# Optimization experiments

Measured on AMD Instinct MI355X. Metric: run time of the kernel, lower is better.

Reference implementation:

```python
import jax, jax.numpy as jnp
import numpy as np

N_TOKEN = 64
H = 16
D = 1024
D_K = 64
D_V = 64
S3 = 30  # 3 * S, number of gated leading positions
GATE_INIT = 10.0


def setup_inputs() -> dict:
    key = jax.random.key(0)
    ks = jax.random.split(key, 8)
    B, L = 32, 2048
    x = jax.random.normal(ks[0], (B, L, D), dtype=jnp.float32)
    q_init = (1.0 / D_K) ** 0.5
    q_tok = jax.random.uniform(ks[1], (1, N_TOKEN, D), minval=-q_init, maxval=q_init, dtype=jnp.float32)
    scale = 0.02
    Wq = jax.random.normal(ks[2], (D, H * D_K), dtype=jnp.float32) * scale
    Wk = jax.random.normal(ks[3], (D, H * D_K), dtype=jnp.float32) * scale
    Wv = jax.random.normal(ks[4], (D, H * D_V), dtype=jnp.float32) * scale
    Wfc = jax.random.normal(ks[5], (H * D_V, D), dtype=jnp.float32) * scale
    gate_logit = -jnp.ones((S3,), dtype=jnp.float32) * GATE_INIT  # matches module init
    gamma = jnp.ones((D,), dtype=jnp.float32)
    beta = jnp.zeros((D,), dtype=jnp.float32)
    return {"x": x, "q_tok": q_tok, "Wq": Wq, "Wk": Wk, "Wv": Wv, "Wfc": Wfc,
            "gate_logit": gate_logit, "gamma": gamma, "beta": beta}


def reference(x, q_tok, Wq, Wk, Wv, Wfc, gate_logit, gamma, beta):
    # x: [B, L, D]; q_tok: [1, n_token, D]. Dropout is identity (eval mode).
    B, L, _ = x.shape
    temp = D_K ** 0.5

    # Cumulative-product gate over the first 30 positions (the torch for-loop).
    gate = jnp.cumprod(1.0 - jax.nn.sigmoid(gate_logit))  # [30]
    x1 = x.at[:, :S3].multiply(gate[None, :, None])

    q = (q_tok @ Wq).reshape(N_TOKEN, H, D_K)          # [n, H, dk]
    k = (x @ Wk).reshape(B, L, H, D_K)                  # [B, L, H, dk]
    v = (x1 @ Wv).reshape(B, L, H, D_V)                 # [B, L, H, dv]

    scores = jnp.einsum('nhd,blhd->bhnl', q / temp, k)  # [B, H, n, L]
    attn = jax.nn.softmax(scores, axis=-1)
    out = jnp.einsum('bhnl,blhd->bnhd', attn, v).reshape(B, N_TOKEN, H * D_V)

    out = out @ Wfc + q_tok                              # residual with query tokens

    # LayerNorm over last dim, eps=1e-6
    mu = jnp.mean(out, axis=-1, keepdims=True)
    var = jnp.mean(jnp.square(out - mu), axis=-1, keepdims=True)
    out = (out - mu) * jax.lax.rsqrt(var + 1e-6) * gamma + beta
    return out
```

## Files before the change

### kernel.cpp

```cpp
#include <hip/hip_runtime.h>
#include <stdint.h>

typedef unsigned short u16;
typedef short bf16x8 __attribute__((ext_vector_type(8)));
typedef float f32x4 __attribute__((ext_vector_type(4)));

__device__ __forceinline__ u16 f2b(float f) {
  uint32_t u = __builtin_bit_cast(uint32_t, f);
  u += 0x7fffu + ((u >> 16) & 1u);
  return (u16)(u >> 16);
}

__device__ __forceinline__ void gload_lds16(const void* g, void* l) {
  __builtin_amdgcn_global_load_lds(
      (const __attribute__((address_space(1))) void*)g,
      (__attribute__((address_space(3))) void*)l, 16, 0, 0);
}

__global__ __launch_bounds__(256) void cvt_kernel(const float* __restrict__ src,
                                                  u16* __restrict__ dst, int n8) {
  int stride = gridDim.x * 256;
  for (int idx = blockIdx.x * 256 + threadIdx.x; idx < n8; idx += stride) {
    int64_t i = (int64_t)idx * 8;
    float4 a = *(const float4*)(src + i);
    float4 b = *(const float4*)(src + i + 4);
    union { u16 u[8]; bf16x8 v; } o;
    o.u[0] = f2b(a.x); o.u[1] = f2b(a.y); o.u[2] = f2b(a.z); o.u[3] = f2b(a.w);
    o.u[4] = f2b(b.x); o.u[5] = f2b(b.y); o.u[6] = f2b(b.z); o.u[7] = f2b(b.w);
    *(bf16x8*)(dst + i) = o.v;
  }
}

__global__ __launch_bounds__(256) void transpose_all_kernel(
    const float* __restrict__ Wk, const float* __restrict__ Wv,
    const float* __restrict__ Wfc, const float* __restrict__ Wq,
    u16* __restrict__ wkvT, u16* __restrict__ wfcT, u16* __restrict__ wqT,
    const float* __restrict__ gl, float* __restrict__ gate) {
  if (blockIdx.x == 0 && threadIdx.x == 0) {
    float g = 1.0f;
    for (int i = 0; i < 30; ++i) {
      float s = 1.0f / (1.0f + __expf(-gl[i]));
      g *= (1.0f - s);
      gate[i] = g;
    }
  }
  __shared__ float ls[64][65];
  int which = blockIdx.x >> 8;
  int tile = blockIdx.x & 255;
  const float* src = (which == 0) ? Wk : (which == 1) ? Wv : (which == 2) ? Wfc : Wq;
  u16* dst = (which == 0) ? wkvT : (which == 1) ? (wkvT + 1024 * 1024)
           : (which == 2) ? wfcT : wqT;
  int t = threadIdx.x;
  int bx = tile & 15;
  int by = tile >> 4;
  int r0 = by * 64, c0 = bx * 64;
  int tr = t >> 6, tc = t & 63;
#pragma unroll
  for (int i = 0; i < 16; ++i)
    ls[tr + i * 4][tc] = src[(int64_t)(r0 + tr + i * 4) * 1024 + c0 + tc];
  __syncthreads();
#pragma unroll
  for (int i = 0; i < 16; ++i)
    dst[(int64_t)(c0 + tr + i * 4) * 1024 + r0 + tc] = f2b(ls[tc][tr + i * 4]);
}

__global__ __launch_bounds__(256, 4) void q_gemm_kernel(
    const u16* __restrict__ qtokb, const u16* __restrict__ wqT, u16* __restrict__ qb) {
  __shared__ u16 As[4096];
  __shared__ u16 Bs[8192];
  int n0 = blockIdx.x * 128;
  int t = threadIdx.x, w = t >> 6, lane = t & 63;
  int wn = w * 32;
  f32x4 acc[2][4] = {};
  int l3 = lane >> 3;
  int colE = ((lane & 7) ^ l3) * 8;
  const u16* aS = qtokb + (int64_t)(w * 16 + l3) * 1024 + colE;
  const u16* bS = wqT + (int64_t)(n0 + w * 32 + l3) * 1024 + colE;
  u16* aD = As + w * 1024;
  u16* bD = Bs + w * 2048;
  int l15 = lane & 15, g16 = lane >> 4;
  for (int kt = 0; kt < 16; ++kt) {
    int ko = kt * 64;
    __syncthreads();
    gload_lds16(aS + ko, aD);
    gload_lds16(aS + ko + 8192, aD + 512);
#pragma unroll
    for (int g = 0; g < 4; ++g) gload_lds16(bS + ko + g * 8192, bD + g * 512);
    __syncthreads();
#pragma unroll
    for (int kk = 0; kk < 2; ++kk) {
      int sl = ((kk * 4 + g16) ^ (l15 & 7)) * 8;
      bf16x8 af[4], bf[2];
#pragma unroll
      for (int j = 0; j < 4; ++j) af[j] = *(const bf16x8*)(As + (j * 16 + l15) * 64 + sl);
#pragma unroll
      for (int i = 0; i < 2; ++i) bf[i] = *(const bf16x8*)(Bs + (wn + i * 16 + l15) * 64 + sl);
#pragma unroll
      for (int i = 0; i < 2; ++i)
#pragma unroll
        for (int j = 0; j < 4; ++j)
          acc[i][j] = __builtin_amdgcn_mfma_f32_16x16x32_bf16(bf[i], af[j], acc[i][j], 0, 0, 0);
    }
  }
  const float sc = 1.44269504f / 8.0f;
  int lr = g16 * 4;
#pragma unroll
  for (int i = 0; i < 2; ++i) {
    int colg = n0 + wn + i * 16 + lr;
#pragma unroll
    for (int j = 0; j < 4; ++j) {
      int qrow = j * 16 + l15;
      u16 p[4];
#pragma unroll
      for (int r = 0; r < 4; ++r) p[r] = f2b(acc[i][j][r] * sc);
      *(uint64_t*)(qb + qrow * 1024 + colg) = *(uint64_t*)p;
    }
  }
}

__global__ __launch_bounds__(256, 3) void kv_gemm_kernel(
    const u16* __restrict__ xb, const u16* __restrict__ wkvT,
    const float* __restrict__ gate, u16* __restrict__ kbuf, u16* __restrict__ vT) {
  __shared__ u16 As[8192];
  __shared__ u16 Bs[8192];
  int d = blockIdx.x;
  int x = d & 7;
  int nb = (d >> 3) & 15;
  int mb = (d >> 7) * 8 + x;
  int m0 = mb * 128, n0 = nb * 128;
  int t = threadIdx.x, w = t >> 6, lane = t & 63;
  int wm = (w >> 1) * 64, wn = (w & 1) * 64;
  bool isV = (n0 >= 1024);
  f32x4 acc[4][4] = {};
  int l3 = lane >> 3;
  int colE = ((lane & 7) ^ l3) * 8;
  const u16* aS = xb + (int64_t)(m0 + w * 32 + l3) * 1024 + colE;
  const u16* bS = wkvT + (int64_t)(n0 + w * 32 + l3) * 1024 + colE;
  u16* aD = As + w * 2048;
  u16* bD = Bs + w * 2048;
  int l15 = lane & 15, g16 = lane >> 4;
  for (int kt = 0; kt < 16; ++kt) {
    int ko = kt * 64;
    __syncthreads();
#pragma unroll
    for (int g = 0; g < 4; ++g) {
      gload_lds16(aS + ko + g * 8192, aD + g * 512);
      gload_lds16(bS + ko + g * 8192, bD + g * 512);
    }
    __syncthreads();
#pragma unroll
    for (int kk = 0; kk < 2; ++kk) {
      int sl = ((kk * 4 + g16) ^ (l15 & 7)) * 8;
      bf16x8 af[4], bf[4];
#pragma unroll
      for (int i = 0; i < 4; ++i) af[i] = *(const bf16x8*)(As + (wm + i * 16 + l15) * 64 + sl);
#pragma unroll
      for (int j = 0; j < 4; ++j) bf[j] = *(const bf16x8*)(Bs + (wn + j * 16 + l15) * 64 + sl);
      if (!isV) {
#pragma unroll
        for (int i = 0; i < 4; ++i)
#pragma unroll
          for (int j = 0; j < 4; ++j)
            acc[i][j] = __builtin_amdgcn_mfma_f32_16x16x32_bf16(bf[i], af[j], acc[i][j], 0, 0, 0);
      } else {
#pragma unroll
        for (int i = 0; i < 4; ++i)
#pragma unroll
          for (int j = 0; j < 4; ++j)
            acc[i][j] = __builtin_amdgcn_mfma_f32_16x16x32_bf16(af[i], bf[j], acc[i][j], 0, 0, 0);
      }
    }
  }
  int b = m0 >> 11, lbase = m0 & 2047;
  int lr = g16 * 4;
  if (!isV) {
#pragma unroll
    for (int i = 0; i < 4; ++i) {
      int dkg = n0 + wn + i * 16 + lr;
      int h = dkg >> 6, dkk = dkg & 63;
#pragma unroll
      for (int j = 0; j < 4; ++j) {
        int l = lbase + wm + j * 16 + l15;
        u16 p[4];
#pragma unroll
        for (int r = 0; r < 4; ++r) p[r] = f2b(acc[i][j][r]);
        *(uint64_t*)(kbuf + ((int64_t)((b * 16 + h) * 2048 + l)) * 64 + dkk) = *(uint64_t*)p;
      }
    }
  } else {
#pragma unroll
    for (int j = 0; j < 4; ++j) {
      int dvg = (n0 - 1024) + wn + j * 16 + l15;
      int h = dvg >> 6, dv = dvg & 63;
#pragma unroll
      for (int i = 0; i < 4; ++i) {
        int lg = lbase + wm + i * 16 + lr;
        u16 p[4];
#pragma unroll
        for (int r = 0; r < 4; ++r) {
          float val = acc[i][j][r];
          int ll = lg + r;
          if (ll < 30) val *= gate[ll];
          p[r] = f2b(val);
        }
        *(uint64_t*)(vT + ((int64_t)((b * 16 + h) * 64 + dv)) * 2048 + lg) = *(uint64_t*)p;
      }
    }
  }
}

__global__ __launch_bounds__(256) void attn_kernel(
    const u16* __restrict__ qb, const u16* __restrict__ kbuf,
    const u16* __restrict__ vT, float* __restrict__ pO,
    float* __restrict__ pm, float* __restrict__ ps) {
  __shared__ u16 Ps[4096];
  int bid = blockIdx.x;
  int b = bid >> 6, h = (bid >> 2) & 15, c = bid & 3;
  int t = threadIdx.x, w = t >> 6, lane = t & 63;
  int l15 = lane & 15, g16 = lane >> 4, lh8 = g16 * 8;
  bf16x8 qf0 = *(const bf16x8*)(qb + (w * 16 + l15) * 1024 + h * 64 + lh8);
  bf16x8 qf1 = *(const bf16x8*)(qb + (w * 16 + l15) * 1024 + h * 64 + 32 + lh8);
  const u16* kB = kbuf + (int64_t)(b * 16 + h) * (2048 * 64);
  const u16* vB = vT + (int64_t)(b * 16 + h) * (64 * 2048);
  char* PsW = (char*)Ps + w * 2048;
  float m_r[4] = {-1e30f, -1e30f, -1e30f, -1e30f};
  float s_r[4] = {0.f, 0.f, 0.f, 0.f};
  f32x4 O[4] = {};
  for (int lt = 0; lt < 8; ++lt) {
    int l0 = c * 512 + lt * 64;
    f32x4 S[4];
#pragma unroll
    for (int ls = 0; ls < 4; ++ls) {
      const u16* kr = kB + (l0 + ls * 16 + l15) * 64 + lh8;
      bf16x8 k0 = *(const bf16x8*)(kr);
      bf16x8 k1 = *(const bf16x8*)(kr + 32);
      f32x4 s = {};
      s = __builtin_amdgcn_mfma_f32_16x16x32_bf16(qf0, k0, s, 0, 0, 0);
      s = __builtin_amdgcn_mfma_f32_16x16x32_bf16(qf1, k1, s, 0, 0, 0);
      S[ls] = s;
    }
    float scale[4];
#pragma unroll
    for (int r = 0; r < 4; ++r) {
      float tm = fmaxf(fmaxf(S[0][r], S[1][r]), fmaxf(S[2][r], S[3][r]));
#pragma unroll
      for (int msk = 1; msk < 16; msk <<= 1)
        tm = fmaxf(tm, __shfl_xor(tm, msk, 16));
      float mn = fmaxf(m_r[r], tm);
      scale[r] = exp2f(m_r[r] - mn);
      m_r[r] = mn;
    }
#pragma unroll
    for (int ls = 0; ls < 4; ++ls)
#pragma unroll
      for (int r = 0; r < 4; ++r) S[ls][r] = exp2f(S[ls][r] - m_r[r]);
#pragma unroll
    for (int r = 0; r < 4; ++r) {
      float psm = (S[0][r] + S[1][r]) + (S[2][r] + S[3][r]);
      s_r[r] = s_r[r] * scale[r] + psm;
    }
#pragma unroll
    for (int ls = 0; ls < 4; ++ls)
#pragma unroll
      for (int r = 0; r < 4; ++r) {
        int row = g16 * 4 + r;
        int off = (ls * 16 + l15) * 2;
        *(u16*)(PsW + row * 128 + (off ^ ((row & 7) << 4))) = f2b(S[ls][r]);
      }
#pragma unroll
    for (int d = 0; d < 4; ++d)
#pragma unroll
      for (int r = 0; r < 4; ++r) O[d][r] *= scale[r];
    bf16x8 pa0, pa1;
    {
      int off0 = g16 * 16;
      pa0 = *(const bf16x8*)(PsW + l15 * 128 + (off0 ^ ((l15 & 7) << 4)));
      pa1 = *(const bf16x8*)(PsW + l15 * 128 + ((off0 + 64) ^ ((l15 & 7) << 4)));
    }
#pragma unroll
    for (int d = 0; d < 4; ++d) {
      const u16* vr = vB + (d * 16 + l15) * 2048 + l0 + lh8;
      bf16x8 v0 = *(const bf16x8*)(vr);
      bf16x8 v1 = *(const bf16x8*)(vr + 32);
      O[d] = __builtin_amdgcn_mfma_f32_16x16x32_bf16(pa0, v0, O[d], 0, 0, 0);
      O[d] = __builtin_amdgcn_mfma_f32_16x16x32_bf16(pa1, v1, O[d], 0, 0, 0);
    }
  }
#pragma unroll
  for (int r = 0; r < 4; ++r) {
    float s = s_r[r];
#pragma unroll
    for (int msk = 1; msk < 16; msk <<= 1) s += __shfl_xor(s, msk, 16);
    s_r[r] = s;
  }
  int64_t pbase = (int64_t)bid * 4096;
#pragma unroll
  for (int d = 0; d < 4; ++d)
#pragma unroll
    for (int r = 0; r < 4; ++r) {
      int n = w * 16 + g16 * 4 + r;
      pO[pbase + n * 64 + d * 16 + l15] = O[d][r];
    }
  if (l15 == 0) {
#pragma unroll
    for (int r = 0; r < 4; ++r) {
      int n = w * 16 + g16 * 4 + r;
      pm[bid * 64 + n] = m_r[r];
      ps[bid * 64 + n] = s_r[r];
    }
  }
}

__global__ __launch_bounds__(256) void attn_combine_kernel(
    const float* __restrict__ pO, const float* __restrict__ pm,
    const float* __restrict__ ps, u16* __restrict__ attnout) {
  int bh = blockIdx.x;
  int b = bh >> 4, h = bh & 15;
  int t = threadIdx.x;
  int dv = t & 63, grp = t >> 6;
#pragma unroll
  for (int i = 0; i < 16; ++i) {
    int n = grp * 16 + i;
    int base = bh * 256 + n;
    float m0 = pm[base], m1 = pm[base + 64], m2 = pm[base + 128], m3 = pm[base + 192];
    float M = fmaxf(fmaxf(m0, m1), fmaxf(m2, m3));
    float w0 = exp2f(m0 - M), w1 = exp2f(m1 - M), w2 = exp2f(m2 - M), w3 = exp2f(m3 - M);
    float stot = w0 * ps[base] + w1 * ps[base + 64] + w2 * ps[base + 128] + w3 * ps[base + 192];
    float inv = 1.0f / stot;
    int64_t ob = (int64_t)bh * 16384 + n * 64 + dv;
    float o = w0 * pO[ob] + w1 * pO[ob + 4096] + w2 * pO[ob + 8192] + w3 * pO[ob + 12288];
    attnout[((int64_t)(b * 64 + n)) * 1024 + h * 64 + dv] = f2b(o * inv);
  }
}

__global__ __launch_bounds__(256, 4) void fc_gemm_kernel(
    const u16* __restrict__ a, const u16* __restrict__ bT,
    const float* __restrict__ q_tok, float* __restrict__ out) {
  __shared__ u16 As[4096];
  __shared__ u16 Bs[8192];
  int m0 = (blockIdx.x >> 3) * 64;
  int n0 = (blockIdx.x & 7) * 128;
  int t = threadIdx.x, w = t >> 6, lane = t & 63;
  int wn = w * 32;
  f32x4 acc[2][4] = {};
  int l3 = lane >> 3;
  int colE = ((lane & 7) ^ l3) * 8;
  const u16* aS = a + (int64_t)(m0 + w * 16 + l3) * 1024 + colE;
  const u16* bS = bT + (int64_t)(n0 + w * 32 + l3) * 1024 + colE;
  u16* aD = As + w * 1024;
  u16* bD = Bs + w * 2048;
  int l15 = lane & 15, g16 = lane >> 4;
  for (int kt = 0; kt < 16; ++kt) {
    int ko = kt * 64;
    __syncthreads();
    gload_lds16(aS + ko, aD);
    gload_lds16(aS + ko + 8192, aD + 512);
#pragma unroll
    for (int g = 0; g < 4; ++g) gload_lds16(bS + ko + g * 8192, bD + g * 512);
    __syncthreads();
#pragma unroll
    for (int kk = 0; kk < 2; ++kk) {
      int sl = ((kk * 4 + g16) ^ (l15 & 7)) * 8;
      bf16x8 af[4], bf[2];
#pragma unroll
      for (int j = 0; j < 4; ++j) af[j] = *(const bf16x8*)(As + (j * 16 + l15) * 64 + sl);
#pragma unroll
      for (int i = 0; i < 2; ++i) bf[i] = *(const bf16x8*)(Bs + (wn + i * 16 + l15) * 64 + sl);
#pragma unroll
      for (int i = 0; i < 2; ++i)
#pragma unroll
        for (int j = 0; j < 4; ++j)
          acc[i][j] = __builtin_amdgcn_mfma_f32_16x16x32_bf16(bf[i], af[j], acc[i][j], 0, 0, 0);
    }
  }
  int lr = g16 * 4;
#pragma unroll
  for (int i = 0; i < 2; ++i) {
    int colg = n0 + wn + i * 16 + lr;
#pragma unroll
    for (int j = 0; j < 4; ++j) {
      int row = m0 + j * 16 + l15;
      float4 res = *(const float4*)(q_tok + (row & 63) * 1024 + colg);
      float4 o;
      o.x = acc[i][j][0] + res.x;
      o.y = acc[i][j][1] + res.y;
      o.z = acc[i][j][2] + res.z;
      o.w = acc[i][j][3] + res.w;
      *(float4*)(out + (int64_t)row * 1024 + colg) = o;
    }
  }
}

__global__ __launch_bounds__(256) void ln_kernel(
    const float* __restrict__ fc, const float* __restrict__ gamma,
    const float* __restrict__ beta, float* __restrict__ out) {
  __shared__ float red[8];
  int row = blockIdx.x, t = threadIdx.x;
  float4 y = *(const float4*)(fc + (int64_t)row * 1024 + t * 4);
  float s = (y.x + y.y) + (y.z + y.w);
  float ss = (y.x * y.x + y.y * y.y) + (y.z * y.z + y.w * y.w);
#pragma unroll
  for (int msk = 1; msk < 64; msk <<= 1) {
    s += __shfl_xor(s, msk, 64);
    ss += __shfl_xor(ss, msk, 64);
  }
  if ((t & 63) == 0) { red[t >> 6] = s; red[4 + (t >> 6)] = ss; }
  __syncthreads();
  s = (red[0] + red[1]) + (red[2] + red[3]);
  ss = (red[4] + red[5]) + (red[6] + red[7]);
  float mu = s * (1.0f / 1024.0f);
  float var = ss * (1.0f / 1024.0f) - mu * mu;
  float rstd = rsqrtf(var + 1e-6f);
  float4 g = *(const float4*)(gamma + t * 4);
  float4 be = *(const float4*)(beta + t * 4);
  float4 o;
  o.x = (y.x - mu) * rstd * g.x + be.x;
  o.y = (y.y - mu) * rstd * g.y + be.y;
  o.z = (y.z - mu) * rstd * g.z + be.z;
  o.w = (y.w - mu) * rstd * g.w + be.w;
  *(float4*)(out + (int64_t)row * 1024 + t * 4) = o;
}

extern "C" void kernel_launch(void* const* d_in, const int* in_sizes, int n_in,
                              void* d_out, int out_size, void* d_ws, size_t ws_size,
                              hipStream_t stream) {
  const float* x     = (const float*)d_in[0];
  const float* q_tok = (const float*)d_in[1];
  const float* Wq    = (const float*)d_in[2];
  const float* Wk    = (const float*)d_in[3];
  const float* Wv    = (const float*)d_in[4];
  const float* Wfc   = (const float*)d_in[5];
  const float* gl    = (const float*)d_in[6];
  const float* gamma = (const float*)d_in[7];
  const float* beta  = (const float*)d_in[8];
  float* out = (float*)d_out;
  char* ws = (char*)d_ws;

  u16*   xb      = (u16*)(ws);
  u16*   kbuf    = (u16*)(ws + 134217728);
  u16*   vT      = (u16*)(ws + 268435456);
  u16*   wkvT    = (u16*)(ws + 402653184);
  u16*   wfcT    = (u16*)(ws + 406847488);
  u16*   wqT     = (u16*)(ws + 408944640);
  u16*   qtokb   = (u16*)(ws + 411041792);
  u16*   qb      = (u16*)(ws + 411172864);
  float* gate    = (float*)(ws + 411303936);
  u16*   attnout = (u16*)(ws + 411304448);
  float* fcout   = (float*)(ws + 415498752);
  float* pO = (float*)(ws);
  float* pm = (float*)(ws + 33554432);
  float* ps = (float*)(ws + 34078720);

  transpose_all_kernel<<<1024, 256, 0, stream>>>(Wk, Wv, Wfc, Wq, wkvT, wfcT, wqT, gl, gate);
  cvt_kernel<<<2048, 256, 0, stream>>>(x, xb, 8388608);
  cvt_kernel<<<32, 256, 0, stream>>>(q_tok, qtokb, 8192);
  q_gemm_kernel<<<8, 256, 0, stream>>>(qtokb, wqT, qb);
  kv_gemm_kernel<<<8192, 256, 0, stream>>>(xb, wkvT, gate, kbuf, vT);
  attn_kernel<<<2048, 256, 0, stream>>>(qb, kbuf, vT, pO, pm, ps);
  attn_combine_kernel<<<512, 256, 0, stream>>>(pO, pm, ps, attnout);
  fc_gemm_kernel<<<256, 256, 0, stream>>>(attnout, wfcT, q_tok, fcout);
  ln_kernel<<<2048, 256, 0, stream>>>(fcout, gamma, beta, out);
}
```

Measured before the change: 682.6 us.

## Fuse fp32-to-bf16 conversion of x into KV GEMM with register prefetch

Removes the separate cvt_kernel pass over x and has kv_gemm_kernel load fp32 x directly. Each tile is converted to bf16 in registers and written to LDS, and the next K-slice is prefetched into registers after the barrier. This drops a full write and read of the 128 MB bf16 copy of x. In exchange each of the 16 N-blocks now reads fp32 x, which is twice the bytes per A-tile load. Register use also rises, so the occupancy hint drops from 3 to 2 blocks per SM.

```diff
diff --git a/kernel.cpp b/kernel.cpp
--- a/kernel.cpp
+++ b/kernel.cpp
@@ -118,15 +118,15 @@
   }
 }
 
-__global__ __launch_bounds__(256, 3) void kv_gemm_kernel(
-    const u16* __restrict__ xb, const u16* __restrict__ wkvT,
+__global__ __launch_bounds__(256, 2) void kv_gemm_kernel(
+    const float* __restrict__ x, const u16* __restrict__ wkvT,
     const float* __restrict__ gate, u16* __restrict__ kbuf, u16* __restrict__ vT) {
   __shared__ u16 As[8192];
   __shared__ u16 Bs[8192];
   int d = blockIdx.x;
-  int x = d & 7;
+  int xc = d & 7;
   int nb = (d >> 3) & 15;
-  int mb = (d >> 7) * 8 + x;
+  int mb = (d >> 7) * 8 + xc;
   int m0 = mb * 128, n0 = nb * 128;
   int t = threadIdx.x, w = t >> 6, lane = t & 63;
   int wm = (w >> 1) * 64, wn = (w & 1) * 64;
@@ -134,20 +134,42 @@
   f32x4 acc[4][4] = {};
   int l3 = lane >> 3;
   int colE = ((lane & 7) ^ l3) * 8;
-  const u16* aS = xb + (int64_t)(m0 + w * 32 + l3) * 1024 + colE;
+  const float* aF = x + (int64_t)(m0 + w * 32 + l3) * 1024 + colE;
   const u16* bS = wkvT + (int64_t)(n0 + w * 32 + l3) * 1024 + colE;
   u16* aD = As + w * 2048;
   u16* bD = Bs + w * 2048;
   int l15 = lane & 15, g16 = lane >> 4;
+  float4 r0a, r0b, r1a, r1b, r2a, r2b, r3a, r3b;
+  r0a = *(const float4*)(aF);             r0b = *(const float4*)(aF + 4);
+  r1a = *(const float4*)(aF + 8192);      r1b = *(const float4*)(aF + 8192 + 4);
+  r2a = *(const float4*)(aF + 16384);     r2b = *(const float4*)(aF + 16384 + 4);
+  r3a = *(const float4*)(aF + 24576);     r3b = *(const float4*)(aF + 24576 + 4);
   for (int kt = 0; kt < 16; ++kt) {
     int ko = kt * 64;
     __syncthreads();
-#pragma unroll
-    for (int g = 0; g < 4; ++g) {
-      gload_lds16(aS + ko + g * 8192, aD + g * 512);
+    {
+      u16 p[8];
+#define CVT_WRITE(g, va, vb)                                                   \
+      p[0] = f2b(va.x); p[1] = f2b(va.y); p[2] = f2b(va.z); p[3] = f2b(va.w);  \
+      p[4] = f2b(vb.x); p[5] = f2b(vb.y); p[6] = f2b(vb.z); p[7] = f2b(vb.w);  \
+      *(bf16x8*)((char*)(aD + (g) * 512) + lane * 16) = *(const bf16x8*)p;
+      CVT_WRITE(0, r0a, r0b)
+      CVT_WRITE(1, r1a, r1b)
+      CVT_WRITE(2, r2a, r2b)
+      CVT_WRITE(3, r3a, r3b)
+#undef CVT_WRITE
+    }
+#pragma unroll
+    for (int g = 0; g < 4; ++g)
       gload_lds16(bS + ko + g * 8192, bD + g * 512);
-    }
-    __syncthreads();
+    __syncthreads();
+    if (kt < 15) {
+      int kn = ko + 64;
+      r0a = *(const float4*)(aF + kn);          r0b = *(const float4*)(aF + kn + 4);
+      r1a = *(const float4*)(aF + kn + 8192);   r1b = *(const float4*)(aF + kn + 8192 + 4);
+      r2a = *(const float4*)(aF + kn + 16384);  r2b = *(const float4*)(aF + kn + 16384 + 4);
+      r3a = *(const float4*)(aF + kn + 24576);  r3b = *(const float4*)(aF + kn + 24576 + 4);
+    }
 #pragma unroll
     for (int kk = 0; kk < 2; ++kk) {
       int sl = ((kk * 4 + g16) ^ (l15 & 7)) * 8;
@@ -436,7 +458,6 @@
   float* out = (float*)d_out;
   char* ws = (char*)d_ws;
 
-  u16*   xb      = (u16*)(ws);
   u16*   kbuf    = (u16*)(ws + 134217728);
   u16*   vT      = (u16*)(ws + 268435456);
   u16*   wkvT    = (u16*)(ws + 402653184);
@@ -452,10 +473,9 @@
   float* ps = (float*)(ws + 34078720);
 
   transpose_all_kernel<<<1024, 256, 0, stream>>>(Wk, Wv, Wfc, Wq, wkvT, wfcT, wqT, gl, gate);
-  cvt_kernel<<<2048, 256, 0, stream>>>(x, xb, 8388608);
   cvt_kernel<<<32, 256, 0, stream>>>(q_tok, qtokb, 8192);
   q_gemm_kernel<<<8, 256, 0, stream>>>(qtokb, wqT, qb);
-  kv_gemm_kernel<<<8192, 256, 0, stream>>>(xb, wkvT, gate, kbuf, vT);
+  kv_gemm_kernel<<<8192, 256, 0, stream>>>(x, wkvT, gate, kbuf, vT);
   attn_kernel<<<2048, 256, 0, stream>>>(qb, kbuf, vT, pO, pm, ps);
   attn_combine_kernel<<<512, 256, 0, stream>>>(pO, pm, ps, attnout);
   fc_gemm_kernel<<<256, 256, 0, stream>>>(attnout, wfcT, q_tok, fcout);
```

After: 647.9 us. -5.1%, faster.
